# Performance work log

Hardware: AMD Instinct MI355X
Metric: run time of the kernel (lower is better)

The kernel has to match this reference:

```python
import jax, jax.numpy as jnp
import numpy as np

IN_FEATURES = 65536
OUT_FEATURES = 262144
NUM_CONNECTIONS = 128


def setup_inputs() -> dict:
    key = jax.random.key(0)
    k1, k2, k3 = jax.random.split(key, 3)
    x = jax.random.normal(k1, (IN_FEATURES,), dtype=jnp.float32)
    connection_indices = jax.random.randint(
        k2, (OUT_FEATURES, NUM_CONNECTIONS), 0, IN_FEATURES, dtype=jnp.int32)
    operator_indices = jax.random.randint(
        k3, (OUT_FEATURES,), 0, 2, dtype=jnp.int32)
    return {"x": x, "connection_indices": connection_indices,
            "operator_indices": operator_indices}


def reference(x, connection_indices, operator_indices):
    # Gather per-output connections: [out_features, num_connections]
    gathered = x[connection_indices]
    mins = jnp.min(gathered, axis=-1)  # fuzzy_min (operator 0)
    maxs = jnp.max(gathered, axis=-1)  # fuzzy_max (operator 1)
    return jnp.where(operator_indices == 0, mins, maxs)
```

## Files before the change

kernel.cpp:

```cpp
#include <hip/hip_runtime.h>
#include <stdint.h>

#define IN_FEATURES 65536
#define OUT_FEATURES 262144
#define NUM_CONN 128
#define BLOCK 1024
#define GRID (OUT_FEATURES / BLOCK)

__global__ __launch_bounds__(BLOCK, 1)
void deep_agg_kernel(const float* __restrict__ x,
                     const int* __restrict__ conn,
                     const int* __restrict__ ops,
                     float* __restrict__ out) {
    __shared__ uint16_t xs[IN_FEATURES];
    const int tid = threadIdx.x;

    const float4* x4 = (const float4*)x;
    #pragma unroll
    for (int k = 0; k < IN_FEATURES / 4 / BLOCK; ++k) {
        int i4 = tid + k * BLOCK;
        float4 v = x4[i4];
        uint32_t a = __float_as_uint(v.x), b = __float_as_uint(v.y);
        uint32_t c = __float_as_uint(v.z), d = __float_as_uint(v.w);
        a += 0x7fffu + ((a >> 16) & 1u);
        b += 0x7fffu + ((b >> 16) & 1u);
        c += 0x7fffu + ((c >> 16) & 1u);
        d += 0x7fffu + ((d >> 16) & 1u);
        uint2 p;
        p.x = (a >> 16) | (b & 0xffff0000u);
        p.y = (c >> 16) | (d & 0xffff0000u);
        ((uint2*)xs)[i4] = p;
    }
    __syncthreads();

    const int o = blockIdx.x * BLOCK + tid;
    const int4* idxp = (const int4*)(conn + (size_t)o * NUM_CONN);
    float mn = 3.4e38f, mx = -3.4e38f;
    #pragma unroll 4
    for (int i = 0; i < NUM_CONN / 4; ++i) {
        int4 v = idxp[i];
        float f0 = __uint_as_float((uint32_t)xs[v.x] << 16);
        float f1 = __uint_as_float((uint32_t)xs[v.y] << 16);
        float f2 = __uint_as_float((uint32_t)xs[v.z] << 16);
        float f3 = __uint_as_float((uint32_t)xs[v.w] << 16);
        mn = fminf(mn, fminf(fminf(f0, f1), fminf(f2, f3)));
        mx = fmaxf(mx, fmaxf(fmaxf(f0, f1), fmaxf(f2, f3)));
    }
    out[o] = (ops[o] == 0) ? mn : mx;
}

extern "C" void kernel_launch(void* const* d_in, const int* in_sizes, int n_in,
                              void* d_out, int out_size, void* d_ws, size_t ws_size,
                              hipStream_t stream) {
    const float* x    = (const float*)d_in[0];
    const int*   conn = (const int*)d_in[1];
    const int*   ops  = (const int*)d_in[2];
    float*       out  = (float*)d_out;
    deep_agg_kernel<<<GRID, BLOCK, 0, stream>>>(x, conn, ops, out);
}
```

Baseline: 203.6 us.

## Coalesce index loads with 16-lane row groups and DPP row reductions

Instead of each thread streaming its own 512-byte index row, every 16-lane group now reads one output's indices cooperatively, so a wave's loads cover contiguous memory. Each lane reduces 8 gathered values, then four DPP row rotations finish the min/max across the 16 lanes. Lane j keeps the result for iteration j, which spreads the per-output write and ops lookup across lanes. This aims to remove the uncoalesced, strided global access to the large index array, at the cost of extra cross-lane DPP instructions and select logic in each iteration.

```diff
diff --git a/kernel.cpp b/kernel.cpp
--- a/kernel.cpp
+++ b/kernel.cpp
@@ -5,7 +5,19 @@
 #define OUT_FEATURES 262144
 #define NUM_CONN 128
 #define BLOCK 1024
-#define GRID (OUT_FEATURES / BLOCK)
+#define WAVES (BLOCK / 64)
+#define OUT_PER_WAVE 64
+#define GRID (OUT_FEATURES / (WAVES * OUT_PER_WAVE))
+
+__device__ __forceinline__ float bf16_widen(uint16_t h) {
+    return __uint_as_float(((uint32_t)h) << 16);
+}
+
+template <int CTRL>
+__device__ __forceinline__ float dpp_mov(float v) {
+    int x = __builtin_amdgcn_update_dpp(0, __float_as_int(v), CTRL, 0xF, 0xF, true);
+    return __int_as_float(x);
+}
 
 __global__ __launch_bounds__(BLOCK, 1)
 void deep_agg_kernel(const float* __restrict__ x,
@@ -33,20 +45,43 @@
     }
     __syncthreads();
 
-    const int o = blockIdx.x * BLOCK + tid;
-    const int4* idxp = (const int4*)(conn + (size_t)o * NUM_CONN);
-    float mn = 3.4e38f, mx = -3.4e38f;
+    const int lane = tid & 63;
+    const int wv   = tid >> 6;
+    const int j    = lane & 15;
+    const int g    = lane >> 4;
+    const int o_base = (blockIdx.x * WAVES + wv) * OUT_PER_WAVE;
+
+    float res_mn = 0.f, res_mx = 0.f;
     #pragma unroll 4
-    for (int i = 0; i < NUM_CONN / 4; ++i) {
-        int4 v = idxp[i];
-        float f0 = __uint_as_float((uint32_t)xs[v.x] << 16);
-        float f1 = __uint_as_float((uint32_t)xs[v.y] << 16);
-        float f2 = __uint_as_float((uint32_t)xs[v.z] << 16);
-        float f3 = __uint_as_float((uint32_t)xs[v.w] << 16);
-        mn = fminf(mn, fminf(fminf(f0, f1), fminf(f2, f3)));
-        mx = fmaxf(mx, fmaxf(fmaxf(f0, f1), fmaxf(f2, f3)));
+    for (int r = 0; r < 16; ++r) {
+        const int o = o_base + 4 * r + g;
+        const int4* p = (const int4*)(conn + (size_t)o * NUM_CONN);
+        int4 v0 = p[j];
+        int4 v1 = p[j + 16];
+
+        float f0 = bf16_widen(xs[v0.x]), f1 = bf16_widen(xs[v0.y]);
+        float f2 = bf16_widen(xs[v0.z]), f3 = bf16_widen(xs[v0.w]);
+        float f4 = bf16_widen(xs[v1.x]), f5 = bf16_widen(xs[v1.y]);
+        float f6 = bf16_widen(xs[v1.z]), f7 = bf16_widen(xs[v1.w]);
+
+        float mn = fminf(fminf(fminf(f0, f1), fminf(f2, f3)),
+                         fminf(fminf(f4, f5), fminf(f6, f7)));
+        float mx = fmaxf(fmaxf(fmaxf(f0, f1), fmaxf(f2, f3)),
+                         fmaxf(fmaxf(f4, f5), fmaxf(f6, f7)));
+
+        mn = fminf(mn, dpp_mov<0x121>(mn));  mx = fmaxf(mx, dpp_mov<0x121>(mx));
+        mn = fminf(mn, dpp_mov<0x122>(mn));  mx = fmaxf(mx, dpp_mov<0x122>(mx));
+        mn = fminf(mn, dpp_mov<0x124>(mn));  mx = fmaxf(mx, dpp_mov<0x124>(mx));
+        mn = fminf(mn, dpp_mov<0x128>(mn));  mx = fmaxf(mx, dpp_mov<0x128>(mx));
+
+        bool keep = (j == r);
+        res_mn = keep ? mn : res_mn;
+        res_mx = keep ? mx : res_mx;
     }
-    out[o] = (ops[o] == 0) ? mn : mx;
+
+    const int oidx = o_base + 4 * j + g;
+    const float result = (ops[oidx] == 0) ? res_mn : res_mx;
+    out[oidx] = result;
 }
 
 extern "C" void kernel_launch(void* const* d_in, const int* in_sizes, int n_in,
```

New measurement: 197.3 us. 3.1% less time.
